# Performance work log

Measured on AMD Instinct MI355X. Metric: run time of the kernel, lower is better.

Reference implementation:

```python
import jax, jax.numpy as jnp
import numpy as np

B, T, V, H, C = 512, 512, 64, 128, 4


def setup_inputs() -> dict:
    key = jax.random.key(0)
    ks = jax.random.split(key, 32)
    s = 0.05  # weight scale
    inp = {
        'x': jax.random.normal(ks[0], (B, T, V), jnp.float32),
        'd': jax.random.uniform(ks[1], (B, T, 1), jnp.float32),
        'm1': (jax.random.uniform(ks[2], (B, T, V)) < 0.5).astype(jnp.float32),
        'h0_1': 0.1 * jax.random.normal(ks[3], (B, H), jnp.float32),
        'h0_2': 0.1 * jax.random.normal(ks[4], (B, H), jnp.float32),
        'h0_3': 0.1 * jax.random.normal(ks[5], (B, H), jnp.float32),
        'W_ih1': s * jax.random.normal(ks[6], (3 * H, V), jnp.float32),
        'W_hh1': s * jax.random.normal(ks[7], (3 * H, H), jnp.float32),
        'b_ih1': jnp.zeros((3 * H,), jnp.float32),
        'b_hh1': jnp.zeros((3 * H,), jnp.float32),
        'W_ih2': s * jax.random.normal(ks[8], (3 * H, H), jnp.float32),
        'W_hh2': s * jax.random.normal(ks[9], (3 * H, H), jnp.float32),
        'b_ih2': jnp.zeros((3 * H,), jnp.float32),
        'b_hh2': jnp.zeros((3 * H,), jnp.float32),
        'W_ih3': s * jax.random.normal(ks[10], (3 * H, H), jnp.float32),
        'W_hh3': s * jax.random.normal(ks[11], (3 * H, H), jnp.float32),
        'b_ih3': jnp.zeros((3 * H,), jnp.float32),
        'b_hh3': jnp.zeros((3 * H,), jnp.float32),
        'W_out': s * jax.random.normal(ks[12], (C, H), jnp.float32),
        'b_out': jax.random.uniform(ks[13], (C,), jnp.float32),
        'W_dx': s * jax.random.normal(ks[14], (V, 1), jnp.float32),
        'b_dx': jax.random.uniform(ks[15], (V,), jnp.float32),
        'W_dh': s * jax.random.normal(ks[16], (H, 1), jnp.float32),
        'b_dh': jax.random.uniform(ks[17], (H,), jnp.float32),
    }
    return inp


def _gru_cell(xt, h, Wih, Whh, bih, bhh):
    # torch.nn.GRUCell math
    gi = xt @ Wih.T + bih          # [B, 3H]
    gh = h @ Whh.T + bhh           # [B, 3H]
    ir, iz, inn = jnp.split(gi, 3, axis=1)
    hr, hz, hn = jnp.split(gh, 3, axis=1)
    r = jax.nn.sigmoid(ir + hr)
    z = jax.nn.sigmoid(iz + hz)
    n = jnp.tanh(inn + r * hn)
    return (1.0 - z) * n + z * h


def reference(x, d, m1, h0_1, h0_2, h0_3,
              W_ih1, W_hh1, b_ih1, b_hh1,
              W_ih2, W_hh2, b_ih2, b_hh2,
              W_ih3, W_hh3, b_ih3, b_hh3,
              W_out, b_out, W_dx, b_dx, W_dh, b_dh):
    x0 = x[:, 0, :]  # first observation used for imputation

    def head(h):
        return jax.nn.softmax(h @ W_out.T + b_out, axis=1)

    # t = 0: no decay, raw input
    h1 = _gru_cell(x0, h0_1, W_ih1, W_hh1, b_ih1, b_hh1)
    h2 = _gru_cell(h1, h0_2, W_ih2, W_hh2, b_ih2, b_hh2)
    h3 = _gru_cell(h2, h0_3, W_ih3, W_hh3, b_ih3, b_hh3)
    y0 = head(h3)

    # time-major scan inputs for t = 1..T-1
    xs = (jnp.swapaxes(x[:, 1:, :], 0, 1),   # x_t
          jnp.swapaxes(x[:, :-1, :], 0, 1),  # x_{t-1}
          jnp.swapaxes(m1[:, 1:, :], 0, 1),  # m_t
          jnp.swapaxes(d[:, 1:, :], 0, 1))   # d_t [T-1, B, 1]

    def step(carry, inp):
        h1, h2, h3 = carry
        xt, xp, mt, dt = inp
        gamma_h = jnp.exp(-jax.nn.relu(dt @ W_dh.T + b_dh))  # [B, H]
        h1 = h1 * gamma_h
        h2 = h2 * gamma_h
        h3 = h3 * gamma_h
        gamma_x = jnp.exp(-jax.nn.relu(dt @ W_dx.T + b_dx))  # [B, V]
        x1 = (xp * gamma_x + (1.0 - gamma_x) * x0) * (1.0 - mt) + mt * xt
        h1 = _gru_cell(x1, h1, W_ih1, W_hh1, b_ih1, b_hh1)
        h2 = _gru_cell(h1, h2, W_ih2, W_hh2, b_ih2, b_hh2)
        h3 = _gru_cell(h2, h3, W_ih3, W_hh3, b_ih3, b_hh3)
        return (h1, h2, h3), head(h3)

    _, ys = jax.lax.scan(step, (h1, h2, h3), xs)  # [T-1, B, C]
    Y = jnp.concatenate([y0[None], ys], axis=0)    # [T, B, C]
    return jnp.swapaxes(Y, 0, 1)                   # [B, T, C]
```

## Files before the change

### kernel.cpp

```cpp
#include <hip/hip_runtime.h>

#define TT 512
#define VV 64
#define RING 16

typedef _Float16 f16;
typedef f16 f16x8 __attribute__((ext_vector_type(8)));
typedef f16 f16x4 __attribute__((ext_vector_type(4)));
typedef float f32x4v __attribute__((ext_vector_type(4)));
typedef unsigned long long u64;
typedef unsigned u32;

#define MFMA(A_,B_,C_) __builtin_amdgcn_mfma_f32_16x16x32_f16((A_),(B_),(C_),0,0,0)
#define AT_LD32(p)   __hip_atomic_load((p), __ATOMIC_RELAXED, __HIP_MEMORY_SCOPE_AGENT)
#define AT_ST32(p,v) __hip_atomic_store((p),(v), __ATOMIC_RELAXED, __HIP_MEMORY_SCOPE_AGENT)
#define AT_LD64(p)   __hip_atomic_load((p), __ATOMIC_RELAXED, __HIP_MEMORY_SCOPE_AGENT)
#define AT_ST64(p,v) __hip_atomic_store((p),(v), __ATOMIC_RELAXED, __HIP_MEMORY_SCOPE_AGENT)

__device__ __forceinline__ void barrier_lds(){ asm volatile("s_waitcnt lgkmcnt(0)\n\ts_barrier" ::: "memory"); }
__device__ __forceinline__ void wait_vm0(){ asm volatile("s_waitcnt vmcnt(0)" ::: "memory"); }
__device__ __forceinline__ float4 ld4(const float* p){ return *(const float4*)p; }

__device__ __forceinline__ f16x8 ldA8(const float* p){
  f16x8 a;
  #pragma unroll
  for (int j = 0; j < 8; ++j) a[j] = (f16)p[j];
  return a;
}

__device__ __forceinline__ int fragOff16(int d0, int b){
  const int kt = d0 >> 5, qq = (d0 >> 3) & 3, j0 = d0 & 7;
  return (kt*64 + qq*16 + b)*8 + j0;
}

__device__ __forceinline__ void fragW_lds(f16x8* buf, int d0, int b, const float* h4){
  f16x4 v;
  #pragma unroll
  for (int e = 0; e < 4; ++e) v[e] = (f16)h4[e];
  *(f16x4*)((f16*)buf + fragOff16(d0, b)) = v;
}

__device__ __forceinline__ void pubFrag(char* slot, int d0, int b, const float* h4){
  union { f16x4 v; u64 u; } uu;
  #pragma unroll
  for (int e = 0; e < 4; ++e) uu.v[e] = (f16)h4[e];
  AT_ST64((u64*)(slot + fragOff16(d0, b)*2), uu.u);
}

__device__ __forceinline__ f16x8 impFrag(const char* slot, int kt, int lane){
  union { u64 u[2]; f16x8 v; } vv;
  const u64* p = (const u64*)(slot + (kt*64 + lane)*16);
  vv.u[0] = AT_LD64((u64*)p);
  vv.u[1] = AT_LD64((u64*)(p + 1));
  return vv.v;
}

__device__ __forceinline__ void spin_ge(u32* f, u32 val){
  if ((threadIdx.x & 63) == 0){
    u32 g = 0;
    while (AT_LD32(f) < val && ++g < (1u << 20)) {}
  }
  asm volatile("" ::: "memory");
}

__device__ __forceinline__ void gates_upd(const f32x4v* Ci, const f32x4v* Ch,
                                          const float* bR, const float* bZ,
                                          const float* bI, const float* bH,
                                          float* hp){
  #pragma unroll
  for (int e = 0; e < 4; ++e){
    float rr = 1.f/(1.f + __expf(-(Ci[0][e] + Ch[0][e] + bR[e])));
    float zz = 1.f/(1.f + __expf(-(Ci[1][e] + Ch[1][e] + bZ[e])));
    float nv = Ci[2][e] + bI[e] + rr*(Ch[2][e] + bH[e]);
    float nn = 1.f - 2.f/(1.f + __expf(2.f*nv));
    hp[e] = (1.f - zz)*nn + zz*hp[e];
  }
}

__global__ void k_init(u32* wsf){
  const int i = blockIdx.x*256 + threadIdx.x;
  if (i < 4096) AT_ST32(wsf + i, 0u);
}

__launch_bounds__(256)
__attribute__((amdgpu_waves_per_eu(1, 1)))
__global__ void k_pipe(const float* __restrict__ x,   const float* __restrict__ dd,
                       const float* __restrict__ m1,
                       const float* __restrict__ h01, const float* __restrict__ h02,
                       const float* __restrict__ h03,
                       const float* __restrict__ Wih1, const float* __restrict__ Whh1,
                       const float* __restrict__ bih1, const float* __restrict__ bhh1,
                       const float* __restrict__ Wih2, const float* __restrict__ Whh2,
                       const float* __restrict__ bih2, const float* __restrict__ bhh2,
                       const float* __restrict__ Wih3, const float* __restrict__ Whh3,
                       const float* __restrict__ bih3, const float* __restrict__ bhh3,
                       const float* __restrict__ Wout, const float* __restrict__ bout,
                       const float* __restrict__ Wdx,  const float* __restrict__ bdx,
                       const float* __restrict__ Wdh,  const float* __restrict__ bdh,
                       float* __restrict__ y, u32* __restrict__ wsf, char* __restrict__ wsd)
{
  __shared__ f16x8 sFrag[2][256];
  __shared__ f16x8 sX1[2][128];
  __shared__ f16x8 sHead[2][256];

  const int tid = threadIdx.x, w = tid >> 6, lane = tid & 63;
  const int q = lane >> 4, r = lane & 15;
  const int blk = blockIdx.x, role = blk >> 5, grp = blk & 31, b0 = grp << 4;

  u32* const FL  = wsf;
  u32* const ACK = wsf + 1024;

#define SLOT(ch,s) (wsd + (size_t)((((ch)*32 + grp)*RING + (s)))*4096)
#define FLP(ch)    (FL  + ((ch)*32 + grp)*16)
#define ACKP(ch)   (ACK + ((ch)*32 + grp)*16)

  const float* bihX = (role == 0) ? bih1 : (role == 1) ? bih2 : bih3;
  const float* bhhX = (role == 0) ? bhh1 : (role == 1) ? bhh2 : bhh3;
  const float* h0X  = (role == 0) ? h01  : (role == 1) ? h02  : h03;

  float bR[2][4], bZ[2][4], bI[2][4], bH[2][4];
  float hS[2][4], WdhL[2][4], bdhL[2][4];
  #pragma unroll
  for (int G = 0; G < 2; ++G){
    const int dG = (w + 4*G)*16 + 4*q;
    #pragma unroll
    for (int e = 0; e < 4; ++e){
      const int d = dG + e;
      bR[G][e] = bihX[d] + bhhX[d];
      bZ[G][e] = bihX[128+d] + bhhX[128+d];
      bI[G][e] = bihX[256+d];
      bH[G][e] = bhhX[256+d];
      WdhL[G][e] = Wdh[d]; bdhL[G][e] = bdh[d];
    }
    float4 a = ld4(h0X + (size_t)(b0+r)*128 + dG);
    hS[G][0]=a.x; hS[G][1]=a.y; hS[G][2]=a.z; hS[G][3]=a.w;
  }
  float dhC = 0.f, dhN = dd[(size_t)(b0+r)*TT + 1];

  if (role == 0){
    f16x8 Ai[2][3][2], Ah[2][3][4];
    #pragma unroll
    for (int G = 0; G < 2; ++G){
      #pragma unroll
      for (int g = 0; g < 3; ++g){
        const int mrow = (g*8 + w + 4*G)*16 + r;
        #pragma unroll
        for (int kt = 0; kt < 2; ++kt) Ai[G][g][kt] = ldA8(Wih1 + mrow*64 + kt*32 + q*8);
        #pragma unroll
        for (int kt = 0; kt < 4; ++kt) Ah[G][g][kt] = ldA8(Whh1 + mrow*128 + kt*32 + q*8);
      }
    }
    const int bx = w*4 + q, v0 = 4*r;
    float Wdx4[4], bdx4[4];
    #pragma unroll
    for (int e = 0; e < 4; ++e){ Wdx4[e] = Wdx[v0+e]; bdx4[e] = bdx[v0+e]; }

    float4 xC = ld4(x + ((size_t)(b0+bx)*TT + 0)*VV + v0);
    const float4 x0v = xC;
    float4 xN = ld4(x  + ((size_t)(b0+bx)*TT + 1)*VV + v0);
    float4 mN = ld4(m1 + ((size_t)(b0+bx)*TT + 1)*VV + v0);
    float dxN = dd[(size_t)(b0+bx)*TT + 1];
    float4 xP = xC, mC = mN; float dxC = dxN;
    __syncthreads();

    for (int t = 0; t < TT; ++t){
      const int par = t & 1;
      if ((t & 3) == 0 && t >= 16) spin_ge(ACKP(0), (u32)(t-13));
      float xi[4];
      if (t == 0){ xi[0]=xC.x; xi[1]=xC.y; xi[2]=xC.z; xi[3]=xC.w; }
      else {
        const float* xc = (const float*)&xC; const float* xp = (const float*)&xP;
        const float* x0e = (const float*)&x0v; const float* me = (const float*)&mC;
        #pragma unroll
        for (int e = 0; e < 4; ++e){
          float gx = __expf(-fmaxf(dxC*Wdx4[e] + bdx4[e], 0.f));
          xi[e] = (xp[e]*gx + (1.f-gx)*x0e[e])*(1.f-me[e]) + me[e]*xc[e];
        }
      }
      fragW_lds(&sX1[par][0], v0, bx, xi);
      #pragma unroll
      for (int G = 0; G < 2; ++G){
        const int dG = (w + 4*G)*16 + 4*q;
        if (t >= 1){
          #pragma unroll
          for (int e = 0; e < 4; ++e)
            hS[G][e] *= __expf(-fmaxf(dhC*WdhL[G][e] + bdhL[G][e], 0.f));
        }
        fragW_lds(&sFrag[par][0], dG, r, hS[G]);
      }
      barrier_lds();
      f16x8 bx1[2], bh4[4];
      #pragma unroll
      for (int kt = 0; kt < 2; ++kt) bx1[kt] = sX1[par][kt*64 + lane];
      #pragma unroll
      for (int kt = 0; kt < 4; ++kt) bh4[kt] = sFrag[par][kt*64 + lane];
      f32x4v Ci[2][3], Ch[2][3];
      #pragma unroll
      for (int G = 0; G < 2; ++G)
        #pragma unroll
        for (int g = 0; g < 3; ++g){ Ci[G][g] = (f32x4v){0,0,0,0}; Ch[G][g] = (f32x4v){0,0,0,0}; }
      #pragma unroll
      for (int G = 0; G < 2; ++G)
        #pragma unroll
        for (int g = 0; g < 3; ++g){
          #pragma unroll
          for (int kt = 0; kt < 4; ++kt) Ch[G][g] = MFMA(Ah[G][g][kt], bh4[kt], Ch[G][g]);
          #pragma unroll
          for (int kt = 0; kt < 2; ++kt) Ci[G][g] = MFMA(Ai[G][g][kt], bx1[kt], Ci[G][g]);
        }
      char* sOut = SLOT(0, t & (RING-1));
      #pragma unroll
      for (int G = 0; G < 2; ++G){
        const int dG = (w + 4*G)*16 + 4*q;
        gates_upd(&Ci[G][0], &Ch[G][0], bR[G], bZ[G], bI[G], bH[G], hS[G]);
        pubFrag(sOut, dG, r, hS[G]);
      }
      if ((t & 3) == 3){
        wait_vm0();
        barrier_lds();
        if (tid == 0) AT_ST32(FLP(0), (u32)(t+1));
      }
      xP = xC; xC = xN; mC = mN; dhC = dhN; dxC = dxN;
      const int tp = (t+2 < TT) ? (t+2) : (TT-1);
      xN  = ld4(x  + ((size_t)(b0+bx)*TT + tp)*VV + v0);
      mN  = ld4(m1 + ((size_t)(b0+bx)*TT + tp)*VV + v0);
      dhN = dd[(size_t)(b0+r)*TT + tp];
      dxN = dd[(size_t)(b0+bx)*TT + tp];
    }
    return;
  }

  {
    const float* Wihp = (role == 1) ? Wih2 : Wih3;
    const float* Whhp = (role == 1) ? Whh2 : Whh3;
    const int cIn = role - 1;

    f16x8 Ai[2][3][4], Ah[2][3][4];
    #pragma unroll
    for (int G = 0; G < 2; ++G){
      #pragma unroll
      for (int g = 0; g < 3; ++g){
        const int mrow = (g*8 + w + 4*G)*16 + r;
        #pragma unroll
        for (int kt = 0; kt < 4; ++kt){
          Ai[G][g][kt] = ldA8(Wihp + mrow*128 + kt*32 + q*8);
          Ah[G][g][kt] = ldA8(Whhp + mrow*128 + kt*32 + q*8);
        }
      }
    }
    f16x8 aO[4]; float bo4[4];
    if (role == 2){
      #pragma unroll
      for (int kt = 0; kt < 4; ++kt){
        f16x8 a;
        #pragma unroll
        for (int j = 0; j < 8; ++j)
          a[j] = (r < 4) ? (f16)Wout[r*128 + kt*32 + q*8 + j] : (f16)0.f;
        aO[kt] = a;
      }
      #pragma unroll
      for (int e = 0; e < 4; ++e) bo4[e] = bout[e];
    }
    __syncthreads();

    spin_ge(FLP(cIn), 8u);
    f16x8 bi[4], biN[4];
    #pragma unroll
    for (int kt = 0; kt < 4; ++kt) bi[kt] = impFrag(SLOT(cIn, 0), kt, lane);

    for (int t = 0; t < TT; ++t){
      const int par = t & 1;
      if (role == 1 && (t & 3) == 0 && t >= 16) spin_ge(ACKP(1), (u32)(t-13));
      if (t + 1 < TT){
        const char* sIn = SLOT(cIn, (t+1) & (RING-1));
        #pragma unroll
        for (int kt = 0; kt < 4; ++kt) biN[kt] = impFrag(sIn, kt, lane);
      }
      #pragma unroll
      for (int G = 0; G < 2; ++G){
        const int dG = (w + 4*G)*16 + 4*q;
        if (t >= 1){
          #pragma unroll
          for (int e = 0; e < 4; ++e)
            hS[G][e] *= __expf(-fmaxf(dhC*WdhL[G][e] + bdhL[G][e], 0.f));
        }
        fragW_lds(&sFrag[par][0], dG, r, hS[G]);
      }
      barrier_lds();
      if (role == 1 && tid == 0) AT_ST32(ACKP(0), (u32)t);
      f16x8 bh4[4];
      #pragma unroll
      for (int kt = 0; kt < 4; ++kt) bh4[kt] = sFrag[par][kt*64 + lane];
      f32x4v Ci[2][3], Ch[2][3];
      #pragma unroll
      for (int G = 0; G < 2; ++G)
        #pragma unroll
        for (int g = 0; g < 3; ++g){ Ci[G][g] = (f32x4v){0,0,0,0}; Ch[G][g] = (f32x4v){0,0,0,0}; }
      #pragma unroll
      for (int G = 0; G < 2; ++G)
        #pragma unroll
        for (int g = 0; g < 3; ++g){
          #pragma unroll
          for (int kt = 0; kt < 4; ++kt) Ch[G][g] = MFMA(Ah[G][g][kt], bh4[kt], Ch[G][g]);
          #pragma unroll
          for (int kt = 0; kt < 4; ++kt) Ci[G][g] = MFMA(Ai[G][g][kt], bi[kt], Ci[G][g]);
        }
      #pragma unroll
      for (int G = 0; G < 2; ++G)
        gates_upd(&Ci[G][0], &Ch[G][0], bR[G], bZ[G], bI[G], bH[G], hS[G]);

      if (role == 1){
        char* sOut = SLOT(1, t & (RING-1));
        #pragma unroll
        for (int G = 0; G < 2; ++G){
          const int dG = (w + 4*G)*16 + 4*q;
          pubFrag(sOut, dG, r, hS[G]);
        }
        if ((t & 3) == 3){
          wait_vm0();
          barrier_lds();
          if (tid == 0) AT_ST32(FLP(1), (u32)(t+1));
          if (t < TT-1) spin_ge(FLP(0), (u32)(t+7 <= TT ? t+7 : TT));
        }
      } else {
        #pragma unroll
        for (int G = 0; G < 2; ++G){
          const int dG = (w + 4*G)*16 + 4*q;
          fragW_lds(&sHead[par][0], dG, r, hS[G]);
        }
        barrier_lds();
        if (tid == 0) AT_ST32(ACKP(1), (u32)(t+1));
        f32x4v cl = {0.f,0.f,0.f,0.f};
        #pragma unroll
        for (int kt = 0; kt < 4; ++kt) cl = MFMA(aO[kt], sHead[par][kt*64 + lane], cl);
        if (tid < 16){
          float l0 = cl[0]+bo4[0], l1 = cl[1]+bo4[1], l2 = cl[2]+bo4[2], l3 = cl[3]+bo4[3];
          float mx = fmaxf(fmaxf(l0,l1), fmaxf(l2,l3));
          float e0 = __expf(l0-mx), e1 = __expf(l1-mx), e2 = __expf(l2-mx), e3 = __expf(l3-mx);
          float inv = 1.f/(e0+e1+e2+e3);
          float4 o; o.x = e0*inv; o.y = e1*inv; o.z = e2*inv; o.w = e3*inv;
          *(float4*)(y + ((size_t)(b0+tid)*TT + t)*4) = o;
        }
        if ((t & 3) == 3 && t < TT-1) spin_ge(FLP(1), (u32)(t+7 <= TT ? t+7 : TT));
      }

      if (t + 1 < TT){
        #pragma unroll
        for (int kt = 0; kt < 4; ++kt) bi[kt] = biN[kt];
      }
      dhC = dhN;
      const int tp = (t+2 < TT) ? (t+2) : (TT-1);
      dhN = dd[(size_t)(b0+r)*TT + tp];
    }
  }
}

extern "C" void kernel_launch(void* const* d_in, const int* in_sizes, int n_in,
                              void* d_out, int out_size, void* d_ws, size_t ws_size,
                              hipStream_t stream) {
  (void)in_sizes; (void)n_in; (void)out_size; (void)ws_size;
  u32*  wsf = (u32*)d_ws;
  char* wsd = (char*)d_ws + 16384;
  k_init<<<dim3(16), dim3(256), 0, stream>>>(wsf);
  k_pipe<<<dim3(96), dim3(256), 0, stream>>>(
      (const float*)d_in[0],  (const float*)d_in[1],  (const float*)d_in[2],
      (const float*)d_in[3],  (const float*)d_in[4],  (const float*)d_in[5],
      (const float*)d_in[6],  (const float*)d_in[7],  (const float*)d_in[8],  (const float*)d_in[9],
      (const float*)d_in[10], (const float*)d_in[11], (const float*)d_in[12], (const float*)d_in[13],
      (const float*)d_in[14], (const float*)d_in[15], (const float*)d_in[16], (const float*)d_in[17],
      (const float*)d_in[18], (const float*)d_in[19],
      (const float*)d_in[20], (const float*)d_in[21],
      (const float*)d_in[22], (const float*)d_in[23],
      (float*)d_out, wsf, wsd);
}
```

Measured before the change: 1.428 ms.

## Coarsen inter-stage flag handoff to 8-step chunks and software-pipeline the head

Stages of the layered GRU pipeline now publish progress flags and acks every 8 timesteps instead of every 4, with a deeper lead (t+17), which cuts global atomic traffic and how often stages spin-wait. Layer 2 acks once per chunk instead of every step. Layer 3 is skewed by one step so the output head for step s-1 runs after the same barrier as step s's recurrence, removing one barrier per step. The atomics are also cast to the global address space so the compiler emits global rather than flat instructions. The cost is more slack in the ring buffer (16 slots with a 16-step lead), which is close to the ring limit and could be a correctness hazard.

```diff
diff --git a/kernel.cpp b/kernel.cpp
--- a/kernel.cpp
+++ b/kernel.cpp
@@ -11,11 +11,14 @@
 typedef unsigned long long u64;
 typedef unsigned u32;
 
+typedef __attribute__((address_space(1))) unsigned gu32;
+typedef __attribute__((address_space(1))) unsigned long long gu64;
+
 #define MFMA(A_,B_,C_) __builtin_amdgcn_mfma_f32_16x16x32_f16((A_),(B_),(C_),0,0,0)
-#define AT_LD32(p)   __hip_atomic_load((p), __ATOMIC_RELAXED, __HIP_MEMORY_SCOPE_AGENT)
-#define AT_ST32(p,v) __hip_atomic_store((p),(v), __ATOMIC_RELAXED, __HIP_MEMORY_SCOPE_AGENT)
-#define AT_LD64(p)   __hip_atomic_load((p), __ATOMIC_RELAXED, __HIP_MEMORY_SCOPE_AGENT)
-#define AT_ST64(p,v) __hip_atomic_store((p),(v), __ATOMIC_RELAXED, __HIP_MEMORY_SCOPE_AGENT)
+#define AT_LD32(p)   __hip_atomic_load((gu32*)(void*)(p), __ATOMIC_RELAXED, __HIP_MEMORY_SCOPE_AGENT)
+#define AT_ST32(p,v) __hip_atomic_store((gu32*)(void*)(p),(v), __ATOMIC_RELAXED, __HIP_MEMORY_SCOPE_AGENT)
+#define AT_LD64(p)   __hip_atomic_load((gu64*)(void*)(p), __ATOMIC_RELAXED, __HIP_MEMORY_SCOPE_AGENT)
+#define AT_ST64(p,v) __hip_atomic_store((gu64*)(void*)(p),(v), __ATOMIC_RELAXED, __HIP_MEMORY_SCOPE_AGENT)
 
 __device__ __forceinline__ void barrier_lds(){ asm volatile("s_waitcnt lgkmcnt(0)\n\ts_barrier" ::: "memory"); }
 __device__ __forceinline__ void wait_vm0(){ asm volatile("s_waitcnt vmcnt(0)" ::: "memory"); }
@@ -165,7 +168,7 @@
 
     for (int t = 0; t < TT; ++t){
       const int par = t & 1;
-      if ((t & 3) == 0 && t >= 16) spin_ge(ACKP(0), (u32)(t-13));
+      if ((t & 7) == 0 && t >= 16) spin_ge(ACKP(0), (u32)(t-8));
       float xi[4];
       if (t == 0){ xi[0]=xC.x; xi[1]=xC.y; xi[2]=xC.z; xi[3]=xC.w; }
       else {
@@ -215,7 +218,7 @@
         gates_upd(&Ci[G][0], &Ch[G][0], bR[G], bZ[G], bI[G], bH[G], hS[G]);
         pubFrag(sOut, dG, r, hS[G]);
       }
-      if ((t & 3) == 3){
+      if ((t & 7) == 7){
         wait_vm0();
         barrier_lds();
         if (tid == 0) AT_ST32(FLP(0), (u32)(t+1));
@@ -230,11 +233,7 @@
     return;
   }
 
-  {
-    const float* Wihp = (role == 1) ? Wih2 : Wih3;
-    const float* Whhp = (role == 1) ? Whh2 : Whh3;
-    const int cIn = role - 1;
-
+  if (role == 1){
     f16x8 Ai[2][3][4], Ah[2][3][4];
     #pragma unroll
     for (int G = 0; G < 2; ++G){
@@ -243,36 +242,23 @@
         const int mrow = (g*8 + w + 4*G)*16 + r;
         #pragma unroll
         for (int kt = 0; kt < 4; ++kt){
-          Ai[G][g][kt] = ldA8(Wihp + mrow*128 + kt*32 + q*8);
-          Ah[G][g][kt] = ldA8(Whhp + mrow*128 + kt*32 + q*8);
-        }
-      }
-    }
-    f16x8 aO[4]; float bo4[4];
-    if (role == 2){
-      #pragma unroll
-      for (int kt = 0; kt < 4; ++kt){
-        f16x8 a;
-        #pragma unroll
-        for (int j = 0; j < 8; ++j)
-          a[j] = (r < 4) ? (f16)Wout[r*128 + kt*32 + q*8 + j] : (f16)0.f;
-        aO[kt] = a;
-      }
-      #pragma unroll
-      for (int e = 0; e < 4; ++e) bo4[e] = bout[e];
+          Ai[G][g][kt] = ldA8(Wih2 + mrow*128 + kt*32 + q*8);
+          Ah[G][g][kt] = ldA8(Whh2 + mrow*128 + kt*32 + q*8);
+        }
+      }
     }
     __syncthreads();
 
-    spin_ge(FLP(cIn), 8u);
+    spin_ge(FLP(0), 16u);
     f16x8 bi[4], biN[4];
     #pragma unroll
-    for (int kt = 0; kt < 4; ++kt) bi[kt] = impFrag(SLOT(cIn, 0), kt, lane);
+    for (int kt = 0; kt < 4; ++kt) bi[kt] = impFrag(SLOT(0, 0), kt, lane);
 
     for (int t = 0; t < TT; ++t){
       const int par = t & 1;
-      if (role == 1 && (t & 3) == 0 && t >= 16) spin_ge(ACKP(1), (u32)(t-13));
+      if ((t & 7) == 0 && t >= 16) spin_ge(ACKP(1), (u32)(t-8));
       if (t + 1 < TT){
-        const char* sIn = SLOT(cIn, (t+1) & (RING-1));
+        const char* sIn = SLOT(0, (t+1) & (RING-1));
         #pragma unroll
         for (int kt = 0; kt < 4; ++kt) biN[kt] = impFrag(sIn, kt, lane);
       }
@@ -287,7 +273,6 @@
         fragW_lds(&sFrag[par][0], dG, r, hS[G]);
       }
       barrier_lds();
-      if (role == 1 && tid == 0) AT_ST32(ACKP(0), (u32)t);
       f16x8 bh4[4];
       #pragma unroll
       for (int kt = 0; kt < 4; ++kt) bh4[kt] = sFrag[par][kt*64 + lane];
@@ -305,31 +290,110 @@
           #pragma unroll
           for (int kt = 0; kt < 4; ++kt) Ci[G][g] = MFMA(Ai[G][g][kt], bi[kt], Ci[G][g]);
         }
-      #pragma unroll
-      for (int G = 0; G < 2; ++G)
+      char* sOut = SLOT(1, t & (RING-1));
+      #pragma unroll
+      for (int G = 0; G < 2; ++G){
+        const int dG = (w + 4*G)*16 + 4*q;
         gates_upd(&Ci[G][0], &Ch[G][0], bR[G], bZ[G], bI[G], bH[G], hS[G]);
-
-      if (role == 1){
-        char* sOut = SLOT(1, t & (RING-1));
+        pubFrag(sOut, dG, r, hS[G]);
+      }
+      if ((t & 7) == 7){
+        wait_vm0();
+        barrier_lds();
+        if (tid == 0){ AT_ST32(FLP(1), (u32)(t+1)); AT_ST32(ACKP(0), (u32)(t+1)); }
+        if (t < TT-1) spin_ge(FLP(0), (u32)(t+17 <= TT ? t+17 : TT));
+      }
+      if (t + 1 < TT){
+        #pragma unroll
+        for (int kt = 0; kt < 4; ++kt) bi[kt] = biN[kt];
+      }
+      dhC = dhN;
+      const int tp = (t+2 < TT) ? (t+2) : (TT-1);
+      dhN = dd[(size_t)(b0+r)*TT + tp];
+    }
+    return;
+  }
+
+  {
+    f16x8 Ai[2][3][4], Ah[2][3][4];
+    #pragma unroll
+    for (int G = 0; G < 2; ++G){
+      #pragma unroll
+      for (int g = 0; g < 3; ++g){
+        const int mrow = (g*8 + w + 4*G)*16 + r;
+        #pragma unroll
+        for (int kt = 0; kt < 4; ++kt){
+          Ai[G][g][kt] = ldA8(Wih3 + mrow*128 + kt*32 + q*8);
+          Ah[G][g][kt] = ldA8(Whh3 + mrow*128 + kt*32 + q*8);
+        }
+      }
+    }
+    f16x8 aO[4]; float bo4[4];
+    #pragma unroll
+    for (int kt = 0; kt < 4; ++kt){
+      f16x8 a;
+      #pragma unroll
+      for (int j = 0; j < 8; ++j)
+        a[j] = (r < 4) ? (f16)Wout[r*128 + kt*32 + q*8 + j] : (f16)0.f;
+      aO[kt] = a;
+    }
+    #pragma unroll
+    for (int e = 0; e < 4; ++e) bo4[e] = bout[e];
+    __syncthreads();
+
+    spin_ge(FLP(1), 16u);
+    f16x8 bi[4], biN[4];
+    #pragma unroll
+    for (int kt = 0; kt < 4; ++kt) bi[kt] = impFrag(SLOT(1, 0), kt, lane);
+
+    for (int s = 0; s <= TT; ++s){
+      const int par = s & 1;
+      #pragma unroll
+      for (int G = 0; G < 2; ++G){
+        const int dG = (w + 4*G)*16 + 4*q;
+        fragW_lds(&sHead[par][0], dG, r, hS[G]);
+      }
+      if (s < TT){
+        if (s + 1 < TT){
+          const char* sIn = SLOT(1, (s+1) & (RING-1));
+          #pragma unroll
+          for (int kt = 0; kt < 4; ++kt) biN[kt] = impFrag(sIn, kt, lane);
+        }
         #pragma unroll
         for (int G = 0; G < 2; ++G){
           const int dG = (w + 4*G)*16 + 4*q;
-          pubFrag(sOut, dG, r, hS[G]);
-        }
-        if ((t & 3) == 3){
-          wait_vm0();
-          barrier_lds();
-          if (tid == 0) AT_ST32(FLP(1), (u32)(t+1));
-          if (t < TT-1) spin_ge(FLP(0), (u32)(t+7 <= TT ? t+7 : TT));
-        }
-      } else {
-        #pragma unroll
-        for (int G = 0; G < 2; ++G){
-          const int dG = (w + 4*G)*16 + 4*q;
-          fragW_lds(&sHead[par][0], dG, r, hS[G]);
-        }
-        barrier_lds();
-        if (tid == 0) AT_ST32(ACKP(1), (u32)(t+1));
+          if (s >= 1){
+            #pragma unroll
+            for (int e = 0; e < 4; ++e)
+              hS[G][e] *= __expf(-fmaxf(dhC*WdhL[G][e] + bdhL[G][e], 0.f));
+          }
+          fragW_lds(&sFrag[par][0], dG, r, hS[G]);
+        }
+      }
+      barrier_lds();
+      if (s < TT){
+        f16x8 bh4[4];
+        #pragma unroll
+        for (int kt = 0; kt < 4; ++kt) bh4[kt] = sFrag[par][kt*64 + lane];
+        f32x4v Ci[2][3], Ch[2][3];
+        #pragma unroll
+        for (int G = 0; G < 2; ++G)
+          #pragma unroll
+          for (int g = 0; g < 3; ++g){ Ci[G][g] = (f32x4v){0,0,0,0}; Ch[G][g] = (f32x4v){0,0,0,0}; }
+        #pragma unroll
+        for (int G = 0; G < 2; ++G)
+          #pragma unroll
+          for (int g = 0; g < 3; ++g){
+            #pragma unroll
+            for (int kt = 0; kt < 4; ++kt) Ch[G][g] = MFMA(Ah[G][g][kt], bh4[kt], Ch[G][g]);
+            #pragma unroll
+            for (int kt = 0; kt < 4; ++kt) Ci[G][g] = MFMA(Ai[G][g][kt], bi[kt], Ci[G][g]);
+          }
+        #pragma unroll
+        for (int G = 0; G < 2; ++G)
+          gates_upd(&Ci[G][0], &Ch[G][0], bR[G], bZ[G], bI[G], bH[G], hS[G]);
+      }
+      if (s >= 1){
         f32x4v cl = {0.f,0.f,0.f,0.f};
         #pragma unroll
         for (int kt = 0; kt < 4; ++kt) cl = MFMA(aO[kt], sHead[par][kt*64 + lane], cl);
@@ -339,17 +403,19 @@
           float e0 = __expf(l0-mx), e1 = __expf(l1-mx), e2 = __expf(l2-mx), e3 = __expf(l3-mx);
           float inv = 1.f/(e0+e1+e2+e3);
           float4 o; o.x = e0*inv; o.y = e1*inv; o.z = e2*inv; o.w = e3*inv;
-          *(float4*)(y + ((size_t)(b0+tid)*TT + t)*4) = o;
-        }
-        if ((t & 3) == 3 && t < TT-1) spin_ge(FLP(1), (u32)(t+7 <= TT ? t+7 : TT));
-      }
-
-      if (t + 1 < TT){
+          *(float4*)(y + ((size_t)(b0+tid)*TT + (s-1))*4) = o;
+        }
+      }
+      if ((s & 7) == 7 && s < TT){
+        if (tid == 0) AT_ST32(ACKP(1), (u32)(s+1));
+        if (s < TT-1) spin_ge(FLP(1), (u32)(s+17 <= TT ? s+17 : TT));
+      }
+      if (s + 1 < TT){
         #pragma unroll
         for (int kt = 0; kt < 4; ++kt) bi[kt] = biN[kt];
       }
       dhC = dhN;
-      const int tp = (t+2 < TT) ? (t+2) : (TT-1);
+      const int tp = (s+2 < TT) ? (s+2) : (TT-1);
       dhN = dd[(size_t)(b0+r)*TT + tp];
     }
   }
```

After: 2.386 ms. 67.0% more time.
